# Optimization experiments

Measured on AMD Instinct MI355X. Metric: run time of the kernel, lower is better.

## Reference

```python
import jax, jax.numpy as jnp
import numpy as np


def dense_image_warp(image, flow):
    """Faithful port of tfa.image.dense_image_warp.

    output[b, y, x, c] = bilinear_sample(image[b], y - flow[b,y,x,0], x - flow[b,y,x,1])
    with floors clamped to [0, size-2] and alphas clamped to [0, 1]
    (matching tfa's _interpolate_bilinear clamping semantics).
    """
    B, H, W, C = image.shape
    gy = jnp.arange(H, dtype=image.dtype)[None, :, None]  # [1,H,1]
    gx = jnp.arange(W, dtype=image.dtype)[None, None, :]  # [1,1,W]
    qy = gy - flow[..., 0]  # [B,H,W]
    qx = gx - flow[..., 1]  # [B,H,W]

    fy = jnp.clip(jnp.floor(qy), 0.0, H - 2)
    fx = jnp.clip(jnp.floor(qx), 0.0, W - 2)
    ay = jnp.clip(qy - fy, 0.0, 1.0)[..., None]  # [B,H,W,1]
    ax = jnp.clip(qx - fx, 0.0, 1.0)[..., None]
    iy = fy.astype(jnp.int32)
    ix = fx.astype(jnp.int32)

    b_idx = jnp.arange(B)[:, None, None]  # [B,1,1]
    top_left = image[b_idx, iy, ix]          # [B,H,W,C]
    top_right = image[b_idx, iy, ix + 1]
    bottom_left = image[b_idx, iy + 1, ix]
    bottom_right = image[b_idx, iy + 1, ix + 1]

    interp_top = top_left + ax * (top_right - top_left)
    interp_bottom = bottom_left + ax * (bottom_right - bottom_left)
    return interp_top + ay * (interp_bottom - interp_top)


def setup_inputs() -> dict:
    key = jax.random.key(0)
    k1, k2 = jax.random.split(key)
    B, H, W, C = 8, 512, 512, 16
    image = jax.random.normal(k1, (B, H, W, C), dtype=jnp.float32)
    flow = jax.random.normal(k2, (B, H, W, 2), dtype=jnp.float32)
    return {"image": image, "flow": flow}


def reference(image, flow):
    return dense_image_warp(image, flow)
```

## Files before the change

kernel.cpp:

```cpp
#include <hip/hip_runtime.h>


__global__ __launch_bounds__(1024) void warp_kernel(
    const float* __restrict__ img,
    const float* __restrict__ flow,
    float* __restrict__ out)
{
    const int bid = blockIdx.x;
    const int logical = ((bid & 7) << 10) + (bid >> 3);

    const int tx = logical & 31;
    const int ty = (logical >> 5) & 31;
    const int b  = logical >> 10;

    const int t  = threadIdx.x;
    const int cg = t & 3;
    const int xx = (t >> 2) & 15;
    const int yy = t >> 6;

    const int x = (tx << 4) + xx;
    const int y = (ty << 4) + yy;

    const int pix = (((b << 9) + y) << 9) + x;

    const float2 f = ((const float2*)flow)[pix];
    const float qy = (float)y - f.x;
    const float qx = (float)x - f.y;

    float fy = floorf(qy); fy = fminf(fmaxf(fy, 0.0f), 510.0f);
    float fx = floorf(qx); fx = fminf(fmaxf(fx, 0.0f), 510.0f);
    const float ay = fminf(fmaxf(qy - fy, 0.0f), 1.0f);
    const float ax = fminf(fmaxf(qx - fx, 0.0f), 1.0f);
    const int iy = (int)fy;
    const int ix = (int)fx;

    const float* p = img + ((size_t)((((b << 9) + iy) << 9) + ix)) * 16 + (cg << 2);

    const float4 tl = *(const float4*)(p);
    const float4 tr = *(const float4*)(p + 16);
    const float4 bl = *(const float4*)(p + 512 * 16);
    const float4 br = *(const float4*)(p + 512 * 16 + 16);

    float4 r;
    {
        float t0, u0;
        t0 = tl.x + ax * (tr.x - tl.x);
        u0 = bl.x + ax * (br.x - bl.x);
        r.x = t0 + ay * (u0 - t0);
        t0 = tl.y + ax * (tr.y - tl.y);
        u0 = bl.y + ax * (br.y - bl.y);
        r.y = t0 + ay * (u0 - t0);
        t0 = tl.z + ax * (tr.z - tl.z);
        u0 = bl.z + ax * (br.z - bl.z);
        r.z = t0 + ay * (u0 - t0);
        t0 = tl.w + ax * (tr.w - tl.w);
        u0 = bl.w + ax * (br.w - bl.w);
        r.w = t0 + ay * (u0 - t0);
    }

    ((float4*)out)[(pix << 2) + cg] = r;
}

extern "C" void kernel_launch(void* const* d_in, const int* in_sizes, int n_in,
                              void* d_out, int out_size, void* d_ws, size_t ws_size,
                              hipStream_t stream) {
    const float* img  = (const float*)d_in[0];
    const float* flow = (const float*)d_in[1];
    float* out = (float*)d_out;

    const int block = 1024;
    const int grid = (8 * 512 * 512 * 4) / block;
    warp_kernel<<<grid, block, 0, stream>>>(img, flow, out);
}
```

Baseline: 243.1 us.

## Load adjacent pixel pairs as contiguous 128B rows and exchange via ds_swizzle

Each 8-lane group now covers two pixels. Every lane loads 16 bytes from a contiguous 128-byte span (the top-left and top-right pixels of one pixel, side by side) for both the top and bottom rows, and the halves are traded between lane pairs with ds_swizzle. The aim is wider, more coalesced gather transactions than separate 64-byte float4 loads per corner. It also drops the 16x16 spatial tiling for linear row-major pixel order and shrinks blocks to 256 threads, which may reduce cache locality. Byte offsets are computed in 32-bit int, which still fits the image size.

New measurement: 240.6 us. No clear change (-1.1%).

```diff
diff --git a/kernel.cpp b/kernel.cpp
--- a/kernel.cpp
+++ b/kernel.cpp
@@ -1,32 +1,37 @@
 #include <hip/hip_runtime.h>
 
 
-__global__ __launch_bounds__(1024) void warp_kernel(
+__device__ __forceinline__ float swz4(float v) {
+    return __int_as_float(__builtin_amdgcn_ds_swizzle(__float_as_int(v), 0x101F));
+}
+__device__ __forceinline__ float4 swz4(float4 v) {
+    float4 r;
+    r.x = swz4(v.x); r.y = swz4(v.y); r.z = swz4(v.z); r.w = swz4(v.w);
+    return r;
+}
+
+__global__ __launch_bounds__(256) void warp_kernel(
     const float* __restrict__ img,
     const float* __restrict__ flow,
     float* __restrict__ out)
 {
-    const int bid = blockIdx.x;
-    const int logical = ((bid & 7) << 10) + (bid >> 3);
+    const int tid  = blockIdx.x * blockDim.x + threadIdx.x;
+    const int lane = threadIdx.x & 63;
+    const int s    = lane & 7;
+    const int q    = (lane >> 3) & 7;
+    const int hi   = (s >> 2) & 1;
+    const int cg   = s & 3;
 
-    const int tx = logical & 31;
-    const int ty = (logical >> 5) & 31;
-    const int b  = logical >> 10;
+    const int pixbase = (tid >> 6) << 4;
+    const int p = pixbase + q + (hi << 3);
 
-    const int t  = threadIdx.x;
-    const int cg = t & 3;
-    const int xx = (t >> 2) & 15;
-    const int yy = t >> 6;
+    const int x = p & 511;
+    const int y = (p >> 9) & 511;
+    const int b = p >> 18;
 
-    const int x = (tx << 4) + xx;
-    const int y = (ty << 4) + yy;
-
-    const int pix = (((b << 9) + y) << 9) + x;
-
-    const float2 f = ((const float2*)flow)[pix];
+    const float2 f = ((const float2*)flow)[p];
     const float qy = (float)y - f.x;
     const float qx = (float)x - f.y;
-
     float fy = floorf(qy); fy = fminf(fmaxf(fy, 0.0f), 510.0f);
     float fx = floorf(qx); fx = fminf(fmaxf(fx, 0.0f), 510.0f);
     const float ay = fminf(fmaxf(qy - fy, 0.0f), 1.0f);
@@ -34,12 +39,28 @@
     const int iy = (int)fy;
     const int ix = (int)fx;
 
-    const float* p = img + ((size_t)((((b << 9) + iy) << 9) + ix)) * 16 + (cg << 2);
+    const int mytop = ((((b << 9) + iy) << 9) + ix) << 6;
+    const int othertop = __builtin_amdgcn_ds_swizzle(mytop, 0x101F);
+    const int top0 = hi ? othertop : mytop;
+    const int top1 = hi ? mytop    : othertop;
 
-    const float4 tl = *(const float4*)(p);
-    const float4 tr = *(const float4*)(p + 16);
-    const float4 bl = *(const float4*)(p + 512 * 16);
-    const float4 br = *(const float4*)(p + 512 * 16 + 16);
+    const char* img8 = (const char*)img;
+    const int so = s << 4;
+
+    const float4 T0 = *(const float4*)(img8 + top0 + so);
+    const float4 T1 = *(const float4*)(img8 + top1 + so);
+    const float4 B0 = *(const float4*)(img8 + top0 + 32768 + so);
+    const float4 B1 = *(const float4*)(img8 + top1 + 32768 + so);
+
+    const float4 sendT = hi ? T0 : T1;
+    const float4 sendB = hi ? B0 : B1;
+    const float4 recvT = swz4(sendT);
+    const float4 recvB = swz4(sendB);
+
+    const float4 tl = hi ? recvT : T0;
+    const float4 tr = hi ? T1    : recvT;
+    const float4 bl = hi ? recvB : B0;
+    const float4 br = hi ? B1    : recvB;
 
     float4 r;
     {
@@ -58,7 +79,7 @@
         r.w = t0 + ay * (u0 - t0);
     }
 
-    ((float4*)out)[(pix << 2) + cg] = r;
+    ((float4*)out)[(p << 2) + cg] = r;
 }
 
 extern "C" void kernel_launch(void* const* d_in, const int* in_sizes, int n_in,
@@ -68,7 +89,8 @@
     const float* flow = (const float*)d_in[1];
     float* out = (float*)d_out;
 
-    const int block = 1024;
-    const int grid = (8 * 512 * 512 * 4) / block;
+    const int total = 8 * 512 * 512 * 4;
+    const int block = 256;
+    const int grid = total / block;
     warp_kernel<<<grid, block, 0, stream>>>(img, flow, out);
 }
```

## Stage image halo tile in shared memory for bilinear gathers

Applied to the files above, without the earlier changes.

Each block cooperatively loads a 28x28-pixel halo region (16 channels) of the image into LDS. The bilinear corner gathers then read from LDS when the sampled location falls inside the halo, and fall back to global memory otherwise. The aim is to replace scattered global gathers with shared-memory reads. In exchange the block loads extra halo data, adds a barrier, and uses about 50 KB of LDS per block, which limits occupancy.

Result: slower. 269.4 us (+10.8%).

```diff
diff --git a/kernel.cpp b/kernel.cpp
--- a/kernel.cpp
+++ b/kernel.cpp
@@ -1,32 +1,37 @@
 #include <hip/hip_runtime.h>
 
+
+#define RAD 6
+#define TS  16
+#define SW  (TS + 2*RAD)
+#define SF4 (SW*SW*4)
 
 __global__ __launch_bounds__(1024) void warp_kernel(
     const float* __restrict__ img,
     const float* __restrict__ flow,
     float* __restrict__ out)
 {
+    __shared__ float4 slab[SF4];
+
     const int bid = blockIdx.x;
     const int logical = ((bid & 7) << 10) + (bid >> 3);
-
     const int tx = logical & 31;
     const int ty = (logical >> 5) & 31;
     const int b  = logical >> 10;
+
+    const int x0 = tx << 4, y0 = ty << 4;
+    const int ox = x0 - RAD, oy = y0 - RAD;
 
     const int t  = threadIdx.x;
     const int cg = t & 3;
     const int xx = (t >> 2) & 15;
     const int yy = t >> 6;
-
-    const int x = (tx << 4) + xx;
-    const int y = (ty << 4) + yy;
-
+    const int x = x0 + xx, y = y0 + yy;
     const int pix = (((b << 9) + y) << 9) + x;
 
     const float2 f = ((const float2*)flow)[pix];
     const float qy = (float)y - f.x;
     const float qx = (float)x - f.y;
-
     float fy = floorf(qy); fy = fminf(fmaxf(fy, 0.0f), 510.0f);
     float fx = floorf(qx); fx = fminf(fmaxf(fx, 0.0f), 510.0f);
     const float ay = fminf(fmaxf(qy - fy, 0.0f), 1.0f);
@@ -34,12 +39,34 @@
     const int iy = (int)fy;
     const int ix = (int)fx;
 
-    const float* p = img + ((size_t)((((b << 9) + iy) << 9) + ix)) * 16 + (cg << 2);
+    const float4* img4 = (const float4*)img;
+    for (int l = t; l < SF4; l += 1024) {
+        const int row = l / (SW * 4);
+        const int u   = l - row * (SW * 4);
+        const int gy  = oy + row;
+        const int gx  = ox + (u >> 2);
+        if ((unsigned)gy < 512u && (unsigned)gx < 512u) {
+            slab[l] = img4[((((((b << 9) + gy) << 9) + gx)) << 2) + (u & 3)];
+        }
+    }
+    __syncthreads();
 
-    const float4 tl = *(const float4*)(p);
-    const float4 tr = *(const float4*)(p + 16);
-    const float4 bl = *(const float4*)(p + 512 * 16);
-    const float4 br = *(const float4*)(p + 512 * 16 + 16);
+    const int ry = iy - oy;
+    const int rx = ix - ox;
+    float4 tl, tr, bl, br;
+    if ((unsigned)ry <= (unsigned)(SW - 2) && (unsigned)rx <= (unsigned)(SW - 2)) {
+        const int s = (ry * SW + rx) * 4 + cg;
+        tl = slab[s];
+        tr = slab[s + 4];
+        bl = slab[s + SW * 4];
+        br = slab[s + SW * 4 + 4];
+    } else {
+        const float* p = img + ((size_t)((((b << 9) + iy) << 9) + ix)) * 16 + (cg << 2);
+        tl = *(const float4*)(p);
+        tr = *(const float4*)(p + 16);
+        bl = *(const float4*)(p + 512 * 16);
+        br = *(const float4*)(p + 512 * 16 + 16);
+    }
 
     float4 r;
     {
```
